# Kernel tuning notes

Hardware: AMD Instinct MI355X
Metric: run time of the kernel (lower is better)

## Reference

```python
import jax, jax.numpy as jnp
import numpy as np

D_IN = 256
D_HID = 256


def prelu(x, a):
    return jnp.maximum(x, 0) + a * jnp.minimum(x, 0)


def setup_inputs() -> dict:
    key = jax.random.key(0)
    ks = jax.random.split(key, 12)
    N, M = 8192, 8192
    s_in = 1.0 / np.sqrt(D_IN)
    s_3in = 1.0 / np.sqrt(3 * D_IN)
    s_half = 1.0 / np.sqrt(D_IN // 2)
    return {
        "anchor": jax.random.normal(ks[0], (N, D_IN), jnp.float32),
        "guess": jax.random.normal(ks[1], (M, D_IN), jnp.float32),
        # w_a: Linear(d_in, d_hid)
        "Wa": jax.random.uniform(ks[2], (D_HID, D_IN), jnp.float32, -s_in, s_in),
        "ba": jax.random.uniform(ks[3], (D_HID,), jnp.float32, -s_in, s_in),
        # w_g: Linear(d_in, d_hid)
        "Wg": jax.random.uniform(ks[4], (D_HID, D_IN), jnp.float32, -s_in, s_in),
        "bg": jax.random.uniform(ks[5], (D_HID,), jnp.float32, -s_in, s_in),
        # w_d: Linear(3*d_in, d_in) -> PReLU -> Linear(d_in, d_in//2) -> PReLU -> Linear(d_in//2, 1)
        "W1": jax.random.uniform(ks[6], (D_IN, 3 * D_IN), jnp.float32, -s_3in, s_3in),
        "b1": jax.random.uniform(ks[7], (D_IN,), jnp.float32, -s_3in, s_3in),
        "a1": jnp.array(0.25, jnp.float32),
        "W2": jax.random.uniform(ks[8], (D_IN // 2, D_IN), jnp.float32, -s_in, s_in),
        "b2": jax.random.uniform(ks[9], (D_IN // 2,), jnp.float32, -s_in, s_in),
        "a2": jnp.array(0.25, jnp.float32),
        "W3": jax.random.uniform(ks[10], (1, D_IN // 2), jnp.float32, -s_half, s_half),
        "b3": jax.random.uniform(ks[11], (1,), jnp.float32, -s_half, s_half),
    }


def reference(anchor, guess, Wa, ba, Wg, bg, W1, b1, a1, W2, b2, a2, W3, b3):
    # projections: [N, d_hid], [M, d_hid]
    ac = anchor @ Wa.T + ba
    ge = guess @ Wg.T + bg
    # unscaled cross-attention: [M, N] score matrix
    score = jax.nn.softmax(ge @ ac.T, axis=-1)
    ge2ac = score @ anchor  # [M, d_in]
    dis_x = jnp.concatenate((guess, ge2ac, guess - ge2ac), axis=-1)  # [M, 3*d_in]
    # dropout is identity in eval mode
    h = prelu(dis_x @ W1.T + b1, a1)
    h = prelu(h @ W2.T + b2, a2)
    return h @ W3.T + b3  # [M, 1]
```

## Files before the change

kernel.cpp:

```cpp
#include <hip/hip_runtime.h>


typedef _Float16 f16;
typedef _Float16 h8_t  __attribute__((ext_vector_type(8)));
typedef _Float16 h4_t  __attribute__((ext_vector_type(4)));
typedef float    f4_t  __attribute__((ext_vector_type(4)));
typedef float    f16x  __attribute__((ext_vector_type(16)));
typedef unsigned int u4_t  __attribute__((ext_vector_type(4)));

#define LOG2E 1.4426950408889634f

__device__ __forceinline__ void llds16(const f16* g, f16* s) {
    __builtin_amdgcn_global_load_lds(
        (const __attribute__((address_space(1))) void*)g,
        (__attribute__((address_space(3))) void*)s, 16, 0, 0);
}
__device__ __forceinline__ unsigned int pk2(float a, float b) {
    auto h = __builtin_amdgcn_cvt_pkrtz(a, b);
    return __builtin_bit_cast(unsigned int, h);
}

__global__ __launch_bounds__(256)
void prep(const float* __restrict__ Wa, const float* __restrict__ Wg,
          const float* __restrict__ W1, const float* __restrict__ W2,
          f16* __restrict__ oa, f16* __restrict__ og,
          f16* __restrict__ o1c, f16* __restrict__ o2)
{
    int i = blockIdx.x * 256 + threadIdx.x;
    if (i < 40960) {
        const float* s; f16* d; int off;
        if (i < 16384)      { s = Wa; d = oa; off = i; }
        else if (i < 32768) { s = Wg; d = og; off = i - 16384; }
        else                { s = W2; d = o2; off = i - 32768; }
        f4_t v = ((const f4_t*)s)[off];
        h4_t h;
        h[0]=(f16)v[0]; h[1]=(f16)v[1]; h[2]=(f16)v[2]; h[3]=(f16)v[3];
        ((h4_t*)d)[off] = h;
    } else {
        int off = i - 40960;
        int j = off >> 7, c0 = (off & 127) * 4;
        const float* r = W1 + (size_t)j * 768;
        f4_t v0, v1;
        if (c0 < 256) { v0 = *(const f4_t*)(r + c0); v1 = *(const f4_t*)(r + 512 + c0); }
        else          { v0 = *(const f4_t*)(r + c0); v1 = *(const f4_t*)(r + 256 + c0); }
        h4_t h;
        #pragma unroll
        for (int e = 0; e < 4; e++)
            h[e] = (f16)(c0 < 256 ? v0[e] + v1[e] : v0[e] - v1[e]);
        ((h4_t*)o1c)[off] = h;
    }
}

__global__ __launch_bounds__(256)
void proj_pair(const float* __restrict__ guess, const float* __restrict__ anchor,
               const f16* __restrict__ WG, const f16* __restrict__ WA,
               const float* __restrict__ bg, const float* __restrict__ ba,
               f16* __restrict__ GE, f16* __restrict__ AC,
               f16* __restrict__ vt)
{
    constexpr int BK = 32, LDA = 40, LDB = 40;
    __shared__ f16 As[64 * LDA];
    __shared__ f16 Bs[128 * LDB];
    const int t = threadIdx.x;
    const int w = t >> 6, l = t & 63, lg = l >> 4, lr = l & 15;
    const int bm = blockIdx.x, bn = blockIdx.y, z = blockIdx.z;
    const float* A   = z ? anchor : guess;
    const f16*   B   = z ? WA : WG;
    const float* bias= z ? ba : bg;
    const float scale= z ? 1.0f : LOG2E;
    f16* C = z ? AC : GE;
    f4_t acc[4][2] = {};

    for (int kt = 0; kt < 256; kt += BK) {
        {
            int row = t >> 2, c8 = (t & 3) * 8;
            const float* Af = A + (size_t)(bm * 64 + row) * 256 + kt + c8;
            f4_t v0 = *(const f4_t*)Af;
            f4_t v1 = *(const f4_t*)(Af + 4);
            h8_t h;
            h[0]=(f16)v0[0]; h[1]=(f16)v0[1]; h[2]=(f16)v0[2]; h[3]=(f16)v0[3];
            h[4]=(f16)v1[0]; h[5]=(f16)v1[1]; h[6]=(f16)v1[2]; h[7]=(f16)v1[3];
            *(h8_t*)(&As[row * LDA + c8]) = h;
        }
        {
            int s0 = t, row = s0 >> 2, c8 = (s0 & 3) * 8;
            *(u4_t*)(&Bs[row * LDB + c8]) =
                *(const u4_t*)(B + (size_t)(bn * 128 + row) * 256 + kt + c8);
            int s1 = t + 256; row = s1 >> 2; c8 = (s1 & 3) * 8;
            *(u4_t*)(&Bs[row * LDB + c8]) =
                *(const u4_t*)(B + (size_t)(bn * 128 + row) * 256 + kt + c8);
        }
        __syncthreads();
        h8_t af[4], bf[2];
        #pragma unroll
        for (int mf = 0; mf < 4; mf++)
            af[mf] = *(const h8_t*)(&As[(mf * 16 + lr) * LDA + lg * 8]);
        #pragma unroll
        for (int nf = 0; nf < 2; nf++)
            bf[nf] = *(const h8_t*)(&Bs[(w * 32 + nf * 16 + lr) * LDB + lg * 8]);
        #pragma unroll
        for (int mf = 0; mf < 4; mf++)
            #pragma unroll
            for (int nf = 0; nf < 2; nf++)
                acc[mf][nf] = __builtin_amdgcn_mfma_f32_16x16x32_f16(
                    af[mf], bf[nf], acc[mf][nf], 0, 0, 0);
        if (z == 1 && bn == 0) {
            const int c = t >> 3, r0 = (t & 7) * 8;
            h8_t h;
            #pragma unroll
            for (int j = 0; j < 8; j++) h[j] = As[(r0 + j) * LDA + c];
            *(h8_t*)(vt + (size_t)(kt + c) * 8192 + bm * 64 + r0) = h;
        }
        __syncthreads();
    }

    #pragma unroll
    for (int mf = 0; mf < 4; mf++)
        #pragma unroll
        for (int nf = 0; nf < 2; nf++)
            #pragma unroll
            for (int r = 0; r < 4; r++) {
                int row = bm * 64 + mf * 16 + lg * 4 + r;
                int col = bn * 128 + w * 32 + nf * 16 + lr;
                C[(size_t)row * 256 + col] = (f16)((acc[mf][nf][r] + bias[col]) * scale);
            }
}

__global__ __launch_bounds__(256, 2)
void flash_attn(const f16* __restrict__ Q, const f16* __restrict__ Kc,
                const f16* __restrict__ Vt, f16* __restrict__ OPN,
                float* __restrict__ mpart, float* __restrict__ lpart)
{
    constexpr int D = 256, BK = 64, NK = 8192, SL = 1024, NT = SL / BK;
    __shared__ f16 Ks[BK * D];
    __shared__ f16 Vs[D * BK];
    const int t = threadIdx.x, w = t >> 6, l = t & 63;
    const int q = l & 31, hi = l >> 5;
    const int sl = blockIdx.x & 7, qb = blockIdx.x >> 3;
    const int k0b = sl * SL;
    const int qg0 = qb * 128 + w * 32;

    h8_t qf[16];
    {
        const f16* qr = Q + (size_t)(qg0 + q) * D + hi * 8;
        #pragma unroll
        for (int ks = 0; ks < 16; ks++) qf[ks] = *(const h8_t*)(qr + ks * 16);
    }

    const int sK0 = ((t & 31) ^ (t >> 5)) << 3;
    const int sx  = (t & 15) ^ (t >> 4);
    const int dV  = (t >> 4) * 2 + (sx >> 3);
    const int cV  = (sx & 7) << 3;

    auto stageK = [&](int k0) {
        #pragma unroll
        for (int i = 0; i < 8; i++) {
            const f16* g = Kc + (size_t)(k0 + i * 8 + (t >> 5)) * D + (sK0 ^ ((i & 1) << 6));
            llds16(g, &Ks[i * 2048 + w * 512]);
        }
    };
    auto stageV = [&](int k0) {
        #pragma unroll
        for (int i = 0; i < 8; i++) {
            const f16* g = Vt + (size_t)(i * 32 + dV) * NK + k0 + cV;
            llds16(g, &Vs[i * 2048 + w * 512]);
        }
    };

    stageK(k0b); stageV(k0b);
    __syncthreads();

    f16x o[8] = {};
    f16x sa0, sa1;
    float m_run = -1e30f, l_run = 0.f;
    const int rswzK = (q & 15) << 4;
    const int kbase0 = q * 512;
    const int vbase  = (q >> 1) * 256;
    const int vswz   = (q >> 1) << 4;
    const int vcol0  = ((q & 1) << 7) | (hi << 4);

    for (int kv = 0; kv < NT; ++kv) {
        #pragma unroll
        for (int r = 0; r < 16; r++) { sa0[r] = 0.f; sa1[r] = 0.f; }
        #pragma unroll
        for (int ks = 0; ks < 16; ks++) {
            const int cb = ((ks * 32) | (hi << 4)) ^ rswzK;
            h8_t a0 = *(const h8_t*)((const char*)Ks + kbase0 + cb);
            h8_t a1 = *(const h8_t*)((const char*)Ks + kbase0 + 16384 + cb);
            sa0 = __builtin_amdgcn_mfma_f32_32x32x16_f16(a0, qf[ks], sa0, 0, 0, 0);
            sa1 = __builtin_amdgcn_mfma_f32_32x32x16_f16(a1, qf[ks], sa1, 0, 0, 0);
        }

        float mt = sa0[0];
        #pragma unroll
        for (int r = 1; r < 16; r++) mt = fmaxf(mt, sa0[r]);
        #pragma unroll
        for (int r = 0; r < 16; r++) mt = fmaxf(mt, sa1[r]);
        mt = fmaxf(mt, __shfl_xor(mt, 32));
        if (!__all(mt <= m_run + 8.0f)) {
            const float mnew = fmaxf(m_run, mt);
            const float corr = exp2f(m_run - mnew);
            #pragma unroll
            for (int r = 0; r < 16; r++) {
                const float c = __shfl(corr, (r & 3) + 8 * (r >> 2) + 4 * hi);
                #pragma unroll
                for (int nb = 0; nb < 8; nb++) o[nb][r] *= c;
            }
            l_run *= corr;
            m_run = mnew;
        }
        float rs = 0.f;
        #pragma unroll
        for (int r = 0; r < 16; r++) { sa0[r] = exp2f(sa0[r] - m_run); rs += sa0[r]; }
        #pragma unroll
        for (int r = 0; r < 16; r++) { sa1[r] = exp2f(sa1[r] - m_run); rs += sa1[r]; }
        rs += __shfl_xor(rs, 32);
        l_run += rs;

        __syncthreads();
        if (kv + 1 < NT) stageK(k0b + (kv + 1) * BK);

        #pragma unroll
        for (int kb = 0; kb < 2; kb++) {
            const f16x& P = kb ? sa1 : sa0;
            #pragma unroll
            for (int s = 0; s < 2; s++) {
                unsigned int w00 = pk2(P[8*s+0], P[8*s+1]);
                unsigned int w01 = pk2(P[8*s+2], P[8*s+3]);
                unsigned int w10 = pk2(P[8*s+4], P[8*s+5]);
                unsigned int w11 = pk2(P[8*s+6], P[8*s+7]);
                asm volatile("v_permlane32_swap_b32 %0, %1" : "+v"(w00), "+v"(w10));
                asm volatile("v_permlane32_swap_b32 %0, %1" : "+v"(w01), "+v"(w11));
                u4_t up; up[0] = w00; up[1] = w01; up[2] = w10; up[3] = w11;
                const h8_t apv = __builtin_bit_cast(h8_t, up);
                const int S = kb * 2 + s;
                const int cb = (vcol0 | (S << 5)) ^ vswz;
                #pragma unroll
                for (int nb = 0; nb < 8; nb++) {
                    h8_t bf = *(const h8_t*)((const char*)Vs + nb * 4096 + vbase + cb);
                    o[nb] = __builtin_amdgcn_mfma_f32_32x32x16_f16(apv, bf, o[nb], 0, 0, 0);
                }
            }
        }
        __syncthreads();
        if (kv + 1 < NT) stageV(k0b + (kv + 1) * BK);
    }

    #pragma unroll
    for (int r = 0; r < 16; r++) {
        const int qr = (r & 3) + 8 * (r >> 2) + 4 * hi;
        const float linv = 1.0f / __shfl(l_run, qr);
        const size_t rowoff = ((size_t)sl * NK + qg0 + qr) * D;
        #pragma unroll
        for (int nb = 0; nb < 8; nb++)
            OPN[rowoff + nb * 32 + q] = (f16)(o[nb][r] * linv);
    }
    if (hi == 0) {
        mpart[(size_t)sl * NK + qg0 + q] = m_run;
        lpart[(size_t)sl * NK + qg0 + q] = l_run;
    }
}

__global__ __launch_bounds__(256)
void mlp1(const float* __restrict__ guess, const f16* __restrict__ OPN,
          const float* __restrict__ mp, const float* __restrict__ lp,
          const f16* __restrict__ W1C, const float* __restrict__ b1,
          const float* __restrict__ a1, f16* __restrict__ H1)
{
    constexpr int LDA = 40, LDB = 40;
    __shared__ f16 As[64 * LDA];
    __shared__ f16 Bs[256 * LDB];
    __shared__ float cn[64][8];
    const int t = threadIdx.x;
    const int w = t >> 6, l = t & 63, lg = l >> 4, lr = l & 15;
    const int m0 = blockIdx.x * 64;

    if (t < 64) {
        float c[8], M = -3.0e38f;
        #pragma unroll
        for (int s = 0; s < 8; s++) { c[s] = mp[s * 8192 + m0 + t]; M = fmaxf(M, c[s]); }
        float wsum = 0.f;
        #pragma unroll
        for (int s = 0; s < 8; s++) { c[s] = exp2f(c[s] - M) * lp[s * 8192 + m0 + t]; wsum += c[s]; }
        const float inv = 1.0f / wsum;
        #pragma unroll
        for (int s = 0; s < 8; s++) cn[t][s] = c[s] * inv;
    }
    __syncthreads();

    const int arow = t >> 2, ac8 = (t & 3) * 8;
    float cnr[8];
    #pragma unroll
    for (int s = 0; s < 8; s++) cnr[s] = cn[arow][s];

    f4_t acc[4][4] = {};
    for (int kt = 0; kt < 512; kt += 32) {
        {
            h8_t h;
            if (kt < 256) {
                const float* Af = guess + (size_t)(m0 + arow) * 256 + kt + ac8;
                f4_t v0 = *(const f4_t*)Af;
                f4_t v1 = *(const f4_t*)(Af + 4);
                h[0]=(f16)v0[0]; h[1]=(f16)v0[1]; h[2]=(f16)v0[2]; h[3]=(f16)v0[3];
                h[4]=(f16)v1[0]; h[5]=(f16)v1[1]; h[6]=(f16)v1[2]; h[7]=(f16)v1[3];
            } else {
                const int d0 = kt - 256 + ac8;
                f4_t v0 = {0.f,0.f,0.f,0.f}, v1 = {0.f,0.f,0.f,0.f};
                #pragma unroll
                for (int s = 0; s < 8; s++) {
                    h8_t ov = *(const h8_t*)(OPN + ((size_t)s * 8192 + m0 + arow) * 256 + d0);
                    const float c = cnr[s];
                    v0[0] += c * (float)ov[0]; v0[1] += c * (float)ov[1];
                    v0[2] += c * (float)ov[2]; v0[3] += c * (float)ov[3];
                    v1[0] += c * (float)ov[4]; v1[1] += c * (float)ov[5];
                    v1[2] += c * (float)ov[6]; v1[3] += c * (float)ov[7];
                }
                h[0]=(f16)v0[0]; h[1]=(f16)v0[1]; h[2]=(f16)v0[2]; h[3]=(f16)v0[3];
                h[4]=(f16)v1[0]; h[5]=(f16)v1[1]; h[6]=(f16)v1[2]; h[7]=(f16)v1[3];
            }
            *(h8_t*)(&As[arow * LDA + ac8]) = h;
        }
        #pragma unroll
        for (int i = 0; i < 4; i++) {
            int s0 = t + i * 256;
            int row = s0 >> 2, c8 = (s0 & 3) * 8;
            *(u4_t*)(&Bs[row * LDB + c8]) =
                *(const u4_t*)(W1C + (size_t)row * 512 + kt + c8);
        }
        __syncthreads();
        h8_t af[4], bf[4];
        #pragma unroll
        for (int mf = 0; mf < 4; mf++)
            af[mf] = *(const h8_t*)(&As[(mf * 16 + lr) * LDA + lg * 8]);
        #pragma unroll
        for (int nf = 0; nf < 4; nf++)
            bf[nf] = *(const h8_t*)(&Bs[(w * 64 + nf * 16 + lr) * LDB + lg * 8]);
        #pragma unroll
        for (int mf = 0; mf < 4; mf++)
            #pragma unroll
            for (int nf = 0; nf < 4; nf++)
                acc[mf][nf] = __builtin_amdgcn_mfma_f32_16x16x32_f16(
                    af[mf], bf[nf], acc[mf][nf], 0, 0, 0);
        __syncthreads();
    }

    const float av = *a1;
    #pragma unroll
    for (int mf = 0; mf < 4; mf++)
        #pragma unroll
        for (int nf = 0; nf < 4; nf++)
            #pragma unroll
            for (int r = 0; r < 4; r++) {
                int row = m0 + mf * 16 + lg * 4 + r;
                int col = w * 64 + nf * 16 + lr;
                float v = acc[mf][nf][r] + b1[col];
                v = v > 0.f ? v : av * v;
                H1[(size_t)row * 256 + col] = (f16)v;
            }
}

__global__ __launch_bounds__(256)
void mlp2_final(const f16* __restrict__ H1, const f16* __restrict__ W216,
                const float* __restrict__ b2, const float* __restrict__ a2,
                const float* __restrict__ W3, const float* __restrict__ b3,
                float* __restrict__ out)
{
    constexpr int LDA = 40, LDB = 40;
    __shared__ f16 As[64 * LDA];
    __shared__ f16 Bs[128 * LDB];
    __shared__ float part[64][68];
    const int t = threadIdx.x;
    const int w = t >> 6, l = t & 63, lg = l >> 4, lr = l & 15;
    const int m0 = blockIdx.x * 64;
    f4_t acc[4][2] = {};

    for (int kt = 0; kt < 256; kt += 32) {
        const int row = t >> 2, c8 = (t & 3) * 8;
        *(u4_t*)(&As[row * LDA + c8]) =
            *(const u4_t*)(H1 + (size_t)(m0 + row) * 256 + kt + c8);
        *(u4_t*)(&Bs[row * LDB + c8]) =
            *(const u4_t*)(W216 + (size_t)row * 256 + kt + c8);
        *(u4_t*)(&Bs[(row + 64) * LDB + c8]) =
            *(const u4_t*)(W216 + (size_t)(row + 64) * 256 + kt + c8);
        __syncthreads();
        h8_t af[4], bf[2];
        #pragma unroll
        for (int mf = 0; mf < 4; mf++)
            af[mf] = *(const h8_t*)(&As[(mf * 16 + lr) * LDA + lg * 8]);
        #pragma unroll
        for (int nf = 0; nf < 2; nf++)
            bf[nf] = *(const h8_t*)(&Bs[(w * 32 + nf * 16 + lr) * LDB + lg * 8]);
        #pragma unroll
        for (int mf = 0; mf < 4; mf++)
            #pragma unroll
            for (int nf = 0; nf < 2; nf++)
                acc[mf][nf] = __builtin_amdgcn_mfma_f32_16x16x32_f16(
                    af[mf], bf[nf], acc[mf][nf], 0, 0, 0);
        __syncthreads();
    }

    const float av = *a2;
    #pragma unroll
    for (int mf = 0; mf < 4; mf++)
        #pragma unroll
        for (int r = 0; r < 4; r++) {
            float p = 0.f;
            #pragma unroll
            for (int nf = 0; nf < 2; nf++) {
                const int col = w * 32 + nf * 16 + lr;
                float v = acc[mf][nf][r] + b2[col];
                v = v > 0.f ? v : av * v;
                p += v * W3[col];
            }
            part[mf * 16 + lg * 4 + r][w * 16 + lr] = p;
        }
    __syncthreads();
    const int row = t >> 2, q4 = t & 3;
    float s2 = 0.f;
    #pragma unroll
    for (int j = 0; j < 16; j++) s2 += part[row][q4 * 16 + j];
    s2 += __shfl_xor(s2, 1);
    s2 += __shfl_xor(s2, 2);
    if (q4 == 0) out[m0 + row] = s2 + b3[0];
}

extern "C" void kernel_launch(void* const* d_in, const int* in_sizes, int n_in,
                              void* d_out, int out_size, void* d_ws, size_t ws_size,
                              hipStream_t stream)
{
    const float* anchor = (const float*)d_in[0];
    const float* guess  = (const float*)d_in[1];
    const float* Wa = (const float*)d_in[2];
    const float* ba = (const float*)d_in[3];
    const float* Wg = (const float*)d_in[4];
    const float* bg = (const float*)d_in[5];
    const float* W1 = (const float*)d_in[6];
    const float* b1 = (const float*)d_in[7];
    const float* a1 = (const float*)d_in[8];
    const float* W2 = (const float*)d_in[9];
    const float* b2 = (const float*)d_in[10];
    const float* a2 = (const float*)d_in[11];
    const float* W3 = (const float*)d_in[12];
    const float* b3 = (const float*)d_in[13];
    float* out = (float*)d_out;
    char* ws = (char*)d_ws;

    const size_t MB = 1u << 20;
    f16* GE16 = (f16*)(ws + 0 * MB);
    f16* AC16 = (f16*)(ws + 4 * MB);
    f16* VT16 = (f16*)(ws + 8 * MB);
    f16* OPN  = (f16*)(ws + 12 * MB);
    f16* WA16 = (f16*)(ws + 44 * MB);
    f16* WG16 = (f16*)(ws + 44 * MB + 128 * 1024);
    f16* W1C  = (f16*)(ws + 44 * MB + 256 * 1024);
    f16* W216 = (f16*)(ws + 44 * MB + 512 * 1024);
    float* MP = (float*)(ws + 45 * MB);
    float* LP = (float*)(ws + 45 * MB + 256 * 1024);
    f16* H1   = (f16*)(ws + 0 * MB);

    prep<<<288, 256, 0, stream>>>(Wa, Wg, W1, W2, WA16, WG16, W1C, W216);

    proj_pair<<<dim3(128, 2, 2), 256, 0, stream>>>(
        guess, anchor, WG16, WA16, bg, ba, GE16, AC16, VT16);

    flash_attn<<<512, 256, 0, stream>>>(GE16, AC16, VT16, OPN, MP, LP);

    mlp1<<<128, 256, 0, stream>>>(guess, OPN, MP, LP, W1C, b1, a1, H1);

    mlp2_final<<<128, 256, 0, stream>>>(H1, W216, b2, a2, W3, b3, out);
}
```

Baseline: 161.2 us.

## Load K and V fragments directly from global memory in flash attention

Removes the LDS staging of K and V tiles (global_load_lds with swizzle) and the block-wide barriers, and has each wave load its MFMA operands straight from global memory, relying on the cache. This drops synchronisation and LDS traffic but makes every wave fetch K/V independently, which raises global/L2 traffic and exposes load latency with no explicit prefetch.

After: 295.9 us. +83.5%, slower.

```diff
diff --git a/kernel.cpp b/kernel.cpp
--- a/kernel.cpp
+++ b/kernel.cpp
@@ -10,11 +10,6 @@
 
 #define LOG2E 1.4426950408889634f
 
-__device__ __forceinline__ void llds16(const f16* g, f16* s) {
-    __builtin_amdgcn_global_load_lds(
-        (const __attribute__((address_space(1))) void*)g,
-        (__attribute__((address_space(3))) void*)s, 16, 0, 0);
-}
 __device__ __forceinline__ unsigned int pk2(float a, float b) {
     auto h = __builtin_amdgcn_cvt_pkrtz(a, b);
     return __builtin_bit_cast(unsigned int, h);
@@ -132,8 +127,6 @@
                 float* __restrict__ mpart, float* __restrict__ lpart)
 {
     constexpr int D = 256, BK = 64, NK = 8192, SL = 1024, NT = SL / BK;
-    __shared__ f16 Ks[BK * D];
-    __shared__ f16 Vs[D * BK];
     const int t = threadIdx.x, w = t >> 6, l = t & 63;
     const int q = l & 31, hi = l >> 5;
     const int sl = blockIdx.x & 7, qb = blockIdx.x >> 3;
@@ -147,46 +140,23 @@
         for (int ks = 0; ks < 16; ks++) qf[ks] = *(const h8_t*)(qr + ks * 16);
     }
 
-    const int sK0 = ((t & 31) ^ (t >> 5)) << 3;
-    const int sx  = (t & 15) ^ (t >> 4);
-    const int dV  = (t >> 4) * 2 + (sx >> 3);
-    const int cV  = (sx & 7) << 3;
-
-    auto stageK = [&](int k0) {
-        #pragma unroll
-        for (int i = 0; i < 8; i++) {
-            const f16* g = Kc + (size_t)(k0 + i * 8 + (t >> 5)) * D + (sK0 ^ ((i & 1) << 6));
-            llds16(g, &Ks[i * 2048 + w * 512]);
-        }
-    };
-    auto stageV = [&](int k0) {
-        #pragma unroll
-        for (int i = 0; i < 8; i++) {
-            const f16* g = Vt + (size_t)(i * 32 + dV) * NK + k0 + cV;
-            llds16(g, &Vs[i * 2048 + w * 512]);
-        }
-    };
-
-    stageK(k0b); stageV(k0b);
-    __syncthreads();
+    const f16* krow = Kc + (size_t)(k0b + q) * D + hi * 8;
+    const f16* vrow = Vt + (size_t)q * NK + k0b + hi * 8;
 
     f16x o[8] = {};
-    f16x sa0, sa1;
     float m_run = -1e30f, l_run = 0.f;
-    const int rswzK = (q & 15) << 4;
-    const int kbase0 = q * 512;
-    const int vbase  = (q >> 1) * 256;
-    const int vswz   = (q >> 1) << 4;
-    const int vcol0  = ((q & 1) << 7) | (hi << 4);
 
     for (int kv = 0; kv < NT; ++kv) {
+        const f16* kp = krow + kv * (BK * D);
+        const f16* vp = vrow + kv * BK;
+
+        f16x sa0, sa1;
         #pragma unroll
         for (int r = 0; r < 16; r++) { sa0[r] = 0.f; sa1[r] = 0.f; }
         #pragma unroll
         for (int ks = 0; ks < 16; ks++) {
-            const int cb = ((ks * 32) | (hi << 4)) ^ rswzK;
-            h8_t a0 = *(const h8_t*)((const char*)Ks + kbase0 + cb);
-            h8_t a1 = *(const h8_t*)((const char*)Ks + kbase0 + 16384 + cb);
+            h8_t a0 = *(const h8_t*)(kp + ks * 16);
+            h8_t a1 = *(const h8_t*)(kp + 32 * D + ks * 16);
             sa0 = __builtin_amdgcn_mfma_f32_32x32x16_f16(a0, qf[ks], sa0, 0, 0, 0);
             sa1 = __builtin_amdgcn_mfma_f32_32x32x16_f16(a1, qf[ks], sa1, 0, 0, 0);
         }
@@ -216,9 +186,6 @@
         for (int r = 0; r < 16; r++) { sa1[r] = exp2f(sa1[r] - m_run); rs += sa1[r]; }
         rs += __shfl_xor(rs, 32);
         l_run += rs;
-
-        __syncthreads();
-        if (kv + 1 < NT) stageK(k0b + (kv + 1) * BK);
 
         #pragma unroll
         for (int kb = 0; kb < 2; kb++) {
@@ -234,16 +201,13 @@
                 u4_t up; up[0] = w00; up[1] = w01; up[2] = w10; up[3] = w11;
                 const h8_t apv = __builtin_bit_cast(h8_t, up);
                 const int S = kb * 2 + s;
-                const int cb = (vcol0 | (S << 5)) ^ vswz;
                 #pragma unroll
                 for (int nb = 0; nb < 8; nb++) {
-                    h8_t bf = *(const h8_t*)((const char*)Vs + nb * 4096 + vbase + cb);
+                    h8_t bf = *(const h8_t*)(vp + (size_t)nb * (32 * NK) + S * 16);
                     o[nb] = __builtin_amdgcn_mfma_f32_32x32x16_f16(apv, bf, o[nb], 0, 0, 0);
                 }
             }
         }
-        __syncthreads();
-        if (kv + 1 < NT) stageV(k0b + (kv + 1) * BK);
     }
 
     #pragma unroll
```

## Process two query tiles per wave and double-buffer K/V in flash attention

Applied to the files above, without the earlier changes.

Each wave now computes 64 query rows (two 32-row tiles) against every K/V tile loaded into shared memory, halving the grid and the K/V traffic per query. K and V staging is double-buffered so the next tile's global-to-LDS loads are issued before computing the current tile, with one barrier per tile instead of two. The cost is roughly doubled accumulator and Q registers, which forces one block per CU and risks spills and lower latency hiding.

New measurement: 457.1 us. +183.5%, slower.

```diff
diff --git a/kernel.cpp b/kernel.cpp
--- a/kernel.cpp
+++ b/kernel.cpp
@@ -126,25 +126,29 @@
             }
 }
 
-__global__ __launch_bounds__(256, 2)
+__global__ __launch_bounds__(256, 1)
 void flash_attn(const f16* __restrict__ Q, const f16* __restrict__ Kc,
                 const f16* __restrict__ Vt, f16* __restrict__ OPN,
                 float* __restrict__ mpart, float* __restrict__ lpart)
 {
     constexpr int D = 256, BK = 64, NK = 8192, SL = 1024, NT = SL / BK;
-    __shared__ f16 Ks[BK * D];
-    __shared__ f16 Vs[D * BK];
+    __shared__ f16 Ks0[BK * D];  __shared__ f16 Vs0[D * BK];
+    __shared__ f16 Ks1[BK * D];  __shared__ f16 Vs1[D * BK];
     const int t = threadIdx.x, w = t >> 6, l = t & 63;
     const int q = l & 31, hi = l >> 5;
     const int sl = blockIdx.x & 7, qb = blockIdx.x >> 3;
     const int k0b = sl * SL;
-    const int qg0 = qb * 128 + w * 32;
-
-    h8_t qf[16];
+    const int qg0 = qb * 256 + w * 64;
+
+    h8_t qfA[16], qfB[16];
     {
-        const f16* qr = Q + (size_t)(qg0 + q) * D + hi * 8;
-        #pragma unroll
-        for (int ks = 0; ks < 16; ks++) qf[ks] = *(const h8_t*)(qr + ks * 16);
+        const f16* qrA = Q + (size_t)(qg0 + q) * D + hi * 8;
+        const f16* qrB = qrA + (size_t)32 * D;
+        #pragma unroll
+        for (int ks = 0; ks < 16; ks++) {
+            qfA[ks] = *(const h8_t*)(qrA + ks * 16);
+            qfB[ks] = *(const h8_t*)(qrB + ks * 16);
+        }
     }
 
     const int sK0 = ((t & 31) ^ (t >> 5)) << 3;
@@ -152,50 +156,36 @@
     const int dV  = (t >> 4) * 2 + (sx >> 3);
     const int cV  = (sx & 7) << 3;
 
-    auto stageK = [&](int k0) {
+    auto stage = [&](int k0, f16* kd, f16* vd) {
         #pragma unroll
         for (int i = 0; i < 8; i++) {
             const f16* g = Kc + (size_t)(k0 + i * 8 + (t >> 5)) * D + (sK0 ^ ((i & 1) << 6));
-            llds16(g, &Ks[i * 2048 + w * 512]);
-        }
-    };
-    auto stageV = [&](int k0) {
+            llds16(g, kd + i * 2048 + w * 512);
+        }
         #pragma unroll
         for (int i = 0; i < 8; i++) {
             const f16* g = Vt + (size_t)(i * 32 + dV) * NK + k0 + cV;
-            llds16(g, &Vs[i * 2048 + w * 512]);
+            llds16(g, vd + i * 2048 + w * 512);
         }
     };
 
-    stageK(k0b); stageV(k0b);
+    stage(k0b, Ks0, Vs0);
     __syncthreads();
 
-    f16x o[8] = {};
-    f16x sa0, sa1;
-    float m_run = -1e30f, l_run = 0.f;
+    f16x oA[8] = {}, oB[8] = {};
+    float mA = -1e30f, lA = 0.f, mB = -1e30f, lB = 0.f;
     const int rswzK = (q & 15) << 4;
     const int kbase0 = q * 512;
     const int vbase  = (q >> 1) * 256;
     const int vswz   = (q >> 1) << 4;
     const int vcol0  = ((q & 1) << 7) | (hi << 4);
 
-    for (int kv = 0; kv < NT; ++kv) {
-        #pragma unroll
-        for (int r = 0; r < 16; r++) { sa0[r] = 0.f; sa1[r] = 0.f; }
-        #pragma unroll
-        for (int ks = 0; ks < 16; ks++) {
-            const int cb = ((ks * 32) | (hi << 4)) ^ rswzK;
-            h8_t a0 = *(const h8_t*)((const char*)Ks + kbase0 + cb);
-            h8_t a1 = *(const h8_t*)((const char*)Ks + kbase0 + 16384 + cb);
-            sa0 = __builtin_amdgcn_mfma_f32_32x32x16_f16(a0, qf[ks], sa0, 0, 0, 0);
-            sa1 = __builtin_amdgcn_mfma_f32_32x32x16_f16(a1, qf[ks], sa1, 0, 0, 0);
-        }
-
-        float mt = sa0[0];
-        #pragma unroll
-        for (int r = 1; r < 16; r++) mt = fmaxf(mt, sa0[r]);
-        #pragma unroll
-        for (int r = 0; r < 16; r++) mt = fmaxf(mt, sa1[r]);
+    auto softmax = [&](f16x& s0, f16x& s1, f16x (&o)[8], float& m_run, float& l_run) {
+        float mt = s0[0];
+        #pragma unroll
+        for (int r = 1; r < 16; r++) mt = fmaxf(mt, s0[r]);
+        #pragma unroll
+        for (int r = 0; r < 16; r++) mt = fmaxf(mt, s1[r]);
         mt = fmaxf(mt, __shfl_xor(mt, 32));
         if (!__all(mt <= m_run + 8.0f)) {
             const float mnew = fmaxf(m_run, mt);
@@ -211,53 +201,91 @@
         }
         float rs = 0.f;
         #pragma unroll
-        for (int r = 0; r < 16; r++) { sa0[r] = exp2f(sa0[r] - m_run); rs += sa0[r]; }
-        #pragma unroll
-        for (int r = 0; r < 16; r++) { sa1[r] = exp2f(sa1[r] - m_run); rs += sa1[r]; }
+        for (int r = 0; r < 16; r++) { s0[r] = exp2f(s0[r] - m_run); rs += s0[r]; }
+        #pragma unroll
+        for (int r = 0; r < 16; r++) { s1[r] = exp2f(s1[r] - m_run); rs += s1[r]; }
         rs += __shfl_xor(rs, 32);
         l_run += rs;
-
-        __syncthreads();
-        if (kv + 1 < NT) stageK(k0b + (kv + 1) * BK);
+    };
+
+    auto tile = [&](int kv, const f16* kr, const f16* vr, f16* kw, f16* vw) {
+        if (kv + 1 < NT) stage(k0b + (kv + 1) * BK, kw, vw);
+
+        f16x sA0, sA1, sB0, sB1;
+        #pragma unroll
+        for (int r = 0; r < 16; r++) { sA0[r]=0.f; sA1[r]=0.f; sB0[r]=0.f; sB1[r]=0.f; }
+        #pragma unroll
+        for (int ks = 0; ks < 16; ks++) {
+            const int cb = ((ks * 32) | (hi << 4)) ^ rswzK;
+            h8_t a0 = *(const h8_t*)((const char*)kr + kbase0 + cb);
+            h8_t a1 = *(const h8_t*)((const char*)kr + kbase0 + 16384 + cb);
+            sA0 = __builtin_amdgcn_mfma_f32_32x32x16_f16(a0, qfA[ks], sA0, 0, 0, 0);
+            sA1 = __builtin_amdgcn_mfma_f32_32x32x16_f16(a1, qfA[ks], sA1, 0, 0, 0);
+            sB0 = __builtin_amdgcn_mfma_f32_32x32x16_f16(a0, qfB[ks], sB0, 0, 0, 0);
+            sB1 = __builtin_amdgcn_mfma_f32_32x32x16_f16(a1, qfB[ks], sB1, 0, 0, 0);
+        }
+
+        softmax(sA0, sA1, oA, mA, lA);
+        softmax(sB0, sB1, oB, mB, lB);
 
         #pragma unroll
         for (int kb = 0; kb < 2; kb++) {
-            const f16x& P = kb ? sa1 : sa0;
+            const f16x& PA = kb ? sA1 : sA0;
+            const f16x& PB = kb ? sB1 : sB0;
             #pragma unroll
             for (int s = 0; s < 2; s++) {
-                unsigned int w00 = pk2(P[8*s+0], P[8*s+1]);
-                unsigned int w01 = pk2(P[8*s+2], P[8*s+3]);
-                unsigned int w10 = pk2(P[8*s+4], P[8*s+5]);
-                unsigned int w11 = pk2(P[8*s+6], P[8*s+7]);
-                asm volatile("v_permlane32_swap_b32 %0, %1" : "+v"(w00), "+v"(w10));
-                asm volatile("v_permlane32_swap_b32 %0, %1" : "+v"(w01), "+v"(w11));
-                u4_t up; up[0] = w00; up[1] = w01; up[2] = w10; up[3] = w11;
-                const h8_t apv = __builtin_bit_cast(h8_t, up);
+                unsigned int a00 = pk2(PA[8*s+0], PA[8*s+1]);
+                unsigned int a01 = pk2(PA[8*s+2], PA[8*s+3]);
+                unsigned int a10 = pk2(PA[8*s+4], PA[8*s+5]);
+                unsigned int a11 = pk2(PA[8*s+6], PA[8*s+7]);
+                asm volatile("v_permlane32_swap_b32 %0, %1" : "+v"(a00), "+v"(a10));
+                asm volatile("v_permlane32_swap_b32 %0, %1" : "+v"(a01), "+v"(a11));
+                u4_t ua; ua[0]=a00; ua[1]=a01; ua[2]=a10; ua[3]=a11;
+                const h8_t apvA = __builtin_bit_cast(h8_t, ua);
+                unsigned int b00 = pk2(PB[8*s+0], PB[8*s+1]);
+                unsigned int b01 = pk2(PB[8*s+2], PB[8*s+3]);
+                unsigned int b10 = pk2(PB[8*s+4], PB[8*s+5]);
+                unsigned int b11 = pk2(PB[8*s+6], PB[8*s+7]);
+                asm volatile("v_permlane32_swap_b32 %0, %1" : "+v"(b00), "+v"(b10));
+                asm volatile("v_permlane32_swap_b32 %0, %1" : "+v"(b01), "+v"(b11));
+                u4_t ub; ub[0]=b00; ub[1]=b01; ub[2]=b10; ub[3]=b11;
+                const h8_t apvB = __builtin_bit_cast(h8_t, ub);
                 const int S = kb * 2 + s;
                 const int cb = (vcol0 | (S << 5)) ^ vswz;
                 #pragma unroll
                 for (int nb = 0; nb < 8; nb++) {
-                    h8_t bf = *(const h8_t*)((const char*)Vs + nb * 4096 + vbase + cb);
-                    o[nb] = __builtin_amdgcn_mfma_f32_32x32x16_f16(apv, bf, o[nb], 0, 0, 0);
+                    h8_t bf = *(const h8_t*)((const char*)vr + nb * 4096 + vbase + cb);
+                    oA[nb] = __builtin_amdgcn_mfma_f32_32x32x16_f16(apvA, bf, oA[nb], 0, 0, 0);
+                    oB[nb] = __builtin_amdgcn_mfma_f32_32x32x16_f16(apvB, bf, oB[nb], 0, 0, 0);
                 }
             }
         }
         __syncthreads();
-        if (kv + 1 < NT) stageV(k0b + (kv + 1) * BK);
-    }
-
-    #pragma unroll
-    for (int r = 0; r < 16; r++) {
-        const int qr = (r & 3) + 8 * (r >> 2) + 4 * hi;
-        const float linv = 1.0f / __shfl(l_run, qr);
-        const size_t rowoff = ((size_t)sl * NK + qg0 + qr) * D;
-        #pragma unroll
-        for (int nb = 0; nb < 8; nb++)
-            OPN[rowoff + nb * 32 + q] = (f16)(o[nb][r] * linv);
-    }
+    };
+
+    for (int kv = 0; kv < NT; kv += 2) {
+        tile(kv,     Ks0, Vs0, Ks1, Vs1);
+        tile(kv + 1, Ks1, Vs1, Ks0, Vs0);
+    }
+
+    auto writeout = [&](const f16x (&o)[8], float l_run, int qoff) {
+        #pragma unroll
+        for (int r = 0; r < 16; r++) {
+            const int qr = (r & 3) + 8 * (r >> 2) + 4 * hi;
+            const float linv = 1.0f / __shfl(l_run, qr);
+            const size_t rowoff = ((size_t)sl * NK + qg0 + qoff + qr) * D;
+            #pragma unroll
+            for (int nb = 0; nb < 8; nb++)
+                OPN[rowoff + nb * 32 + q] = (f16)(o[nb][r] * linv);
+        }
+    };
+    writeout(oA, lA, 0);
+    writeout(oB, lB, 32);
     if (hi == 0) {
-        mpart[(size_t)sl * NK + qg0 + q] = m_run;
-        lpart[(size_t)sl * NK + qg0 + q] = l_run;
+        mpart[(size_t)sl * NK + qg0 + q] = mA;
+        lpart[(size_t)sl * NK + qg0 + q] = lA;
+        mpart[(size_t)sl * NK + qg0 + 32 + q] = mB;
+        lpart[(size_t)sl * NK + qg0 + 32 + q] = lB;
     }
 }
 
@@ -463,7 +491,7 @@
     proj_pair<<<dim3(128, 2, 2), 256, 0, stream>>>(
         guess, anchor, WG16, WA16, bg, ba, GE16, AC16, VT16);
 
-    flash_attn<<<512, 256, 0, stream>>>(GE16, AC16, VT16, OPN, MP, LP);
+    flash_attn<<<256, 256, 0, stream>>>(GE16, AC16, VT16, OPN, MP, LP);
 
     mlp1<<<128, 256, 0, stream>>>(guess, OPN, MP, LP, W1C, b1, a1, H1);
 
```

## Fuse MLP layers into one kernel and widen projection tiles to full width

Applied to the files above, without the earlier changes.

Merges the two MLP kernels so the first hidden activation stays in shared memory instead of going through global memory, and removes one launch. Shared memory is reused through a carved arena. The projection kernel now computes all 256 output columns per block, halving A-tile loads and conversion work but halving the grid. The transpose of V is now done by every anchor block.

New measurement: 158.8 us. About the same (-1.5%).

```diff
diff --git a/kernel.cpp b/kernel.cpp
--- a/kernel.cpp
+++ b/kernel.cpp
@@ -58,20 +58,20 @@
                f16* __restrict__ GE, f16* __restrict__ AC,
                f16* __restrict__ vt)
 {
-    constexpr int BK = 32, LDA = 40, LDB = 40;
+    constexpr int LDA = 40, LDB = 40;
     __shared__ f16 As[64 * LDA];
-    __shared__ f16 Bs[128 * LDB];
+    __shared__ f16 Bs[256 * LDB];
     const int t = threadIdx.x;
     const int w = t >> 6, l = t & 63, lg = l >> 4, lr = l & 15;
-    const int bm = blockIdx.x, bn = blockIdx.y, z = blockIdx.z;
+    const int bm = blockIdx.x, z = blockIdx.y;
     const float* A   = z ? anchor : guess;
     const f16*   B   = z ? WA : WG;
     const float* bias= z ? ba : bg;
     const float scale= z ? 1.0f : LOG2E;
     f16* C = z ? AC : GE;
-    f4_t acc[4][2] = {};
-
-    for (int kt = 0; kt < 256; kt += BK) {
+    f4_t acc[4][4] = {};
+
+    for (int kt = 0; kt < 256; kt += 32) {
         {
             int row = t >> 2, c8 = (t & 3) * 8;
             const float* Af = A + (size_t)(bm * 64 + row) * 256 + kt + c8;
@@ -82,29 +82,28 @@
             h[4]=(f16)v1[0]; h[5]=(f16)v1[1]; h[6]=(f16)v1[2]; h[7]=(f16)v1[3];
             *(h8_t*)(&As[row * LDA + c8]) = h;
         }
-        {
-            int s0 = t, row = s0 >> 2, c8 = (s0 & 3) * 8;
+        #pragma unroll
+        for (int i = 0; i < 4; i++) {
+            int s0 = t + i * 256;
+            int row = s0 >> 2, c8 = (s0 & 3) * 8;
             *(u4_t*)(&Bs[row * LDB + c8]) =
-                *(const u4_t*)(B + (size_t)(bn * 128 + row) * 256 + kt + c8);
-            int s1 = t + 256; row = s1 >> 2; c8 = (s1 & 3) * 8;
-            *(u4_t*)(&Bs[row * LDB + c8]) =
-                *(const u4_t*)(B + (size_t)(bn * 128 + row) * 256 + kt + c8);
-        }
-        __syncthreads();
-        h8_t af[4], bf[2];
+                *(const u4_t*)(B + (size_t)row * 256 + kt + c8);
+        }
+        __syncthreads();
+        h8_t af[4], bf[4];
         #pragma unroll
         for (int mf = 0; mf < 4; mf++)
             af[mf] = *(const h8_t*)(&As[(mf * 16 + lr) * LDA + lg * 8]);
         #pragma unroll
-        for (int nf = 0; nf < 2; nf++)
-            bf[nf] = *(const h8_t*)(&Bs[(w * 32 + nf * 16 + lr) * LDB + lg * 8]);
-        #pragma unroll
-        for (int mf = 0; mf < 4; mf++)
-            #pragma unroll
-            for (int nf = 0; nf < 2; nf++)
+        for (int nf = 0; nf < 4; nf++)
+            bf[nf] = *(const h8_t*)(&Bs[(w * 64 + nf * 16 + lr) * LDB + lg * 8]);
+        #pragma unroll
+        for (int mf = 0; mf < 4; mf++)
+            #pragma unroll
+            for (int nf = 0; nf < 4; nf++)
                 acc[mf][nf] = __builtin_amdgcn_mfma_f32_16x16x32_f16(
                     af[mf], bf[nf], acc[mf][nf], 0, 0, 0);
-        if (z == 1 && bn == 0) {
+        if (z == 1) {
             const int c = t >> 3, r0 = (t & 7) * 8;
             h8_t h;
             #pragma unroll
@@ -117,11 +116,11 @@
     #pragma unroll
     for (int mf = 0; mf < 4; mf++)
         #pragma unroll
-        for (int nf = 0; nf < 2; nf++)
+        for (int nf = 0; nf < 4; nf++)
             #pragma unroll
             for (int r = 0; r < 4; r++) {
                 int row = bm * 64 + mf * 16 + lg * 4 + r;
-                int col = bn * 128 + w * 32 + nf * 16 + lr;
+                int col = w * 64 + nf * 16 + lr;
                 C[(size_t)row * 256 + col] = (f16)((acc[mf][nf][r] + bias[col]) * scale);
             }
 }
@@ -262,15 +261,23 @@
 }
 
 __global__ __launch_bounds__(256)
-void mlp1(const float* __restrict__ guess, const f16* __restrict__ OPN,
-          const float* __restrict__ mp, const float* __restrict__ lp,
-          const f16* __restrict__ W1C, const float* __restrict__ b1,
-          const float* __restrict__ a1, f16* __restrict__ H1)
+void mlp_fused(const float* __restrict__ guess, const f16* __restrict__ OPN,
+               const float* __restrict__ mp, const float* __restrict__ lp,
+               const f16* __restrict__ W1C, const float* __restrict__ b1,
+               const float* __restrict__ a1, const f16* __restrict__ W216,
+               const float* __restrict__ b2, const float* __restrict__ a2,
+               const float* __restrict__ W3, const float* __restrict__ b3,
+               float* __restrict__ out)
 {
-    constexpr int LDA = 40, LDB = 40;
-    __shared__ f16 As[64 * LDA];
-    __shared__ f16 Bs[256 * LDB];
-    __shared__ float cn[64][8];
+    constexpr int LDA = 40, LDB = 40, LDH = 264;
+    __shared__ __align__(16) char arena[61440];
+    f16* As  = (f16*)arena;
+    f16* Bs1 = (f16*)(arena + 5120);
+    float (*cn)[8] = (float(*)[8])(arena + 25600);
+    f16* H1s = (f16*)arena;
+    f16* Bs2 = (f16*)(arena + 33792);
+    float (*part)[68] = (float(*)[68])(arena + 44032);
+
     const int t = threadIdx.x;
     const int w = t >> 6, l = t & 63, lg = l >> 4, lr = l & 15;
     const int m0 = blockIdx.x * 64;
@@ -324,7 +331,7 @@
         for (int i = 0; i < 4; i++) {
             int s0 = t + i * 256;
             int row = s0 >> 2, c8 = (s0 & 3) * 8;
-            *(u4_t*)(&Bs[row * LDB + c8]) =
+            *(u4_t*)(&Bs1[row * LDB + c8]) =
                 *(const u4_t*)(W1C + (size_t)row * 512 + kt + c8);
         }
         __syncthreads();
@@ -334,7 +341,7 @@
             af[mf] = *(const h8_t*)(&As[(mf * 16 + lr) * LDA + lg * 8]);
         #pragma unroll
         for (int nf = 0; nf < 4; nf++)
-            bf[nf] = *(const h8_t*)(&Bs[(w * 64 + nf * 16 + lr) * LDB + lg * 8]);
+            bf[nf] = *(const h8_t*)(&Bs1[(w * 64 + nf * 16 + lr) * LDB + lg * 8]);
         #pragma unroll
         for (int mf = 0; mf < 4; mf++)
             #pragma unroll
@@ -344,72 +351,57 @@
         __syncthreads();
     }
 
-    const float av = *a1;
+    {
+        const float av = *a1;
+        #pragma unroll
+        for (int mf = 0; mf < 4; mf++)
+            #pragma unroll
+            for (int nf = 0; nf < 4; nf++)
+                #pragma unroll
+                for (int r = 0; r < 4; r++) {
+                    int row = mf * 16 + lg * 4 + r;
+                    int col = w * 64 + nf * 16 + lr;
+                    float v = acc[mf][nf][r] + b1[col];
+                    v = v > 0.f ? v : av * v;
+                    H1s[row * LDH + col] = (f16)v;
+                }
+    }
+
+    f4_t acc2[4][2] = {};
+    for (int kt = 0; kt < 256; kt += 32) {
+        const int row = t >> 2, c8 = (t & 3) * 8;
+        *(u4_t*)(&Bs2[row * LDB + c8]) =
+            *(const u4_t*)(W216 + (size_t)row * 256 + kt + c8);
+        *(u4_t*)(&Bs2[(row + 64) * LDB + c8]) =
+            *(const u4_t*)(W216 + (size_t)(row + 64) * 256 + kt + c8);
+        __syncthreads();
+        h8_t af[4], bf[2];
+        #pragma unroll
+        for (int mf = 0; mf < 4; mf++)
+            af[mf] = *(const h8_t*)(&H1s[(mf * 16 + lr) * LDH + kt + lg * 8]);
+        #pragma unroll
+        for (int nf = 0; nf < 2; nf++)
+            bf[nf] = *(const h8_t*)(&Bs2[(w * 32 + nf * 16 + lr) * LDB + lg * 8]);
+        #pragma unroll
+        for (int mf = 0; mf < 4; mf++)
+            #pragma unroll
+            for (int nf = 0; nf < 2; nf++)
+                acc2[mf][nf] = __builtin_amdgcn_mfma_f32_16x16x32_f16(
+                    af[mf], bf[nf], acc2[mf][nf], 0, 0, 0);
+        __syncthreads();
+    }
+
+    const float av2 = *a2;
     #pragma unroll
     for (int mf = 0; mf < 4; mf++)
         #pragma unroll
-        for (int nf = 0; nf < 4; nf++)
-            #pragma unroll
-            for (int r = 0; r < 4; r++) {
-                int row = m0 + mf * 16 + lg * 4 + r;
-                int col = w * 64 + nf * 16 + lr;
-                float v = acc[mf][nf][r] + b1[col];
-                v = v > 0.f ? v : av * v;
-                H1[(size_t)row * 256 + col] = (f16)v;
-            }
-}
-
-__global__ __launch_bounds__(256)
-void mlp2_final(const f16* __restrict__ H1, const f16* __restrict__ W216,
-                const float* __restrict__ b2, const float* __restrict__ a2,
-                const float* __restrict__ W3, const float* __restrict__ b3,
-                float* __restrict__ out)
-{
-    constexpr int LDA = 40, LDB = 40;
-    __shared__ f16 As[64 * LDA];
-    __shared__ f16 Bs[128 * LDB];
-    __shared__ float part[64][68];
-    const int t = threadIdx.x;
-    const int w = t >> 6, l = t & 63, lg = l >> 4, lr = l & 15;
-    const int m0 = blockIdx.x * 64;
-    f4_t acc[4][2] = {};
-
-    for (int kt = 0; kt < 256; kt += 32) {
-        const int row = t >> 2, c8 = (t & 3) * 8;
-        *(u4_t*)(&As[row * LDA + c8]) =
-            *(const u4_t*)(H1 + (size_t)(m0 + row) * 256 + kt + c8);
-        *(u4_t*)(&Bs[row * LDB + c8]) =
-            *(const u4_t*)(W216 + (size_t)row * 256 + kt + c8);
-        *(u4_t*)(&Bs[(row + 64) * LDB + c8]) =
-            *(const u4_t*)(W216 + (size_t)(row + 64) * 256 + kt + c8);
-        __syncthreads();
-        h8_t af[4], bf[2];
-        #pragma unroll
-        for (int mf = 0; mf < 4; mf++)
-            af[mf] = *(const h8_t*)(&As[(mf * 16 + lr) * LDA + lg * 8]);
-        #pragma unroll
-        for (int nf = 0; nf < 2; nf++)
-            bf[nf] = *(const h8_t*)(&Bs[(w * 32 + nf * 16 + lr) * LDB + lg * 8]);
-        #pragma unroll
-        for (int mf = 0; mf < 4; mf++)
-            #pragma unroll
-            for (int nf = 0; nf < 2; nf++)
-                acc[mf][nf] = __builtin_amdgcn_mfma_f32_16x16x32_f16(
-                    af[mf], bf[nf], acc[mf][nf], 0, 0, 0);
-        __syncthreads();
-    }
-
-    const float av = *a2;
-    #pragma unroll
-    for (int mf = 0; mf < 4; mf++)
-        #pragma unroll
         for (int r = 0; r < 4; r++) {
             float p = 0.f;
             #pragma unroll
             for (int nf = 0; nf < 2; nf++) {
                 const int col = w * 32 + nf * 16 + lr;
-                float v = acc[mf][nf][r] + b2[col];
-                v = v > 0.f ? v : av * v;
+                float v = acc2[mf][nf][r] + b2[col];
+                v = v > 0.f ? v : av2 * v;
                 p += v * W3[col];
             }
             part[mf * 16 + lg * 4 + r][w * 16 + lr] = p;
@@ -456,16 +448,14 @@
     f16* W216 = (f16*)(ws + 44 * MB + 512 * 1024);
     float* MP = (float*)(ws + 45 * MB);
     float* LP = (float*)(ws + 45 * MB + 256 * 1024);
-    f16* H1   = (f16*)(ws + 0 * MB);
 
     prep<<<288, 256, 0, stream>>>(Wa, Wg, W1, W2, WA16, WG16, W1C, W216);
 
-    proj_pair<<<dim3(128, 2, 2), 256, 0, stream>>>(
+    proj_pair<<<dim3(128, 2), 256, 0, stream>>>(
         guess, anchor, WG16, WA16, bg, ba, GE16, AC16, VT16);
 
     flash_attn<<<512, 256, 0, stream>>>(GE16, AC16, VT16, OPN, MP, LP);
 
-    mlp1<<<128, 256, 0, stream>>>(guess, OPN, MP, LP, W1C, b1, a1, H1);
-
-    mlp2_final<<<128, 256, 0, stream>>>(H1, W216, b2, a2, W3, b3, out);
-}
+    mlp_fused<<<128, 256, 0, stream>>>(guess, OPN, MP, LP, W1C, b1, a1,
+                                       W216, b2, a2, W3, b3, out);
+}
```
